# Kernel tuning notes

Measured on AMD Instinct MI355X. Metric: run time of the kernel, lower is better.

Reference implementation:

```python
import jax, jax.numpy as jnp
import numpy as np

N = 1_048_576   # collocation points
D_IN = 3        # seq_net[0]
H = 32          # hidden width (seq_net[1..3])
B = 4           # seq_net[-1] = number of parallel branches / outputs


def setup_inputs() -> dict:
    key = jax.random.key(0)
    ks = jax.random.split(key, 9)

    def init_w(k, shape, fan_in):
        bound = 1.0 / np.sqrt(fan_in)
        return jax.random.uniform(k, shape, jnp.float32, -bound, bound)

    x = jax.random.normal(ks[0], (N, D_IN), dtype=jnp.float32)
    # Per-branch weights stacked on leading branch axis B (torch.nn.Linear init ranges).
    W0 = init_w(ks[1], (B, D_IN, H), D_IN)
    b0 = init_w(ks[2], (B, H), D_IN)
    W1 = init_w(ks[3], (B, H, H), H)
    b1 = init_w(ks[4], (B, H), H)
    W2 = init_w(ks[5], (B, H, H), H)
    b2 = init_w(ks[6], (B, H), H)
    W3 = init_w(ks[7], (B, H, 1), H)
    b3 = init_w(ks[8], (B, 1), H)
    return {"x": x, "W0": W0, "b0": b0, "W1": W1, "b1": b1,
            "W2": W2, "b2": b2, "W3": W3, "b3": b3}


def reference(x, W0, b0, W1, b1, W2, b2, W3, b3):
    # All B branches computed as one batched GEMM chain (same math as the
    # python loop over per-branch Linear+tanh stacks in PFNN.forward).
    h = jnp.tanh(jnp.einsum('nd,bdh->bnh', x, W0) + b0[:, None, :])   # [B,N,H]
    h = jnp.tanh(jnp.einsum('bnd,bdh->bnh', h, W1) + b1[:, None, :])  # [B,N,H]
    h = jnp.tanh(jnp.einsum('bnd,bdh->bnh', h, W2) + b2[:, None, :])  # [B,N,H]
    out = jnp.einsum('bnd,bdh->bnh', h, W3) + b3[:, None, :]          # [B,N,1]
    # torch.cat(preds, dim=1): branch outputs side by side -> [N, B]
    return jnp.transpose(out[:, :, 0])
```

## Files before the change

kernel.cpp:

```cpp
#include <hip/hip_runtime.h>


#define NPTS 1048576
#define BLOCK 256
#define HROW 72
#define SCALE 2.8853900817779268f

#define OFF_BSC  16384
#define OFF_W0S  17408
#define OFF_B0S  18944
#define OFF_W3P  19456

using f16   = _Float16;
using f16x8 = __attribute__((ext_vector_type(8))) _Float16;
using f32x4 = __attribute__((ext_vector_type(4))) float;
using hfx2  = decltype(__builtin_amdgcn_cvt_pkrtz(0.0f, 0.0f));

__device__ __forceinline__ void tanh4_pre(float v0, float v1, float v2, float v3,
                                          float& o0, float& o1, float& o2, float& o3)
{
    float a0 = __builtin_amdgcn_exp2f(v0) + 1.0f;
    float a1 = __builtin_amdgcn_exp2f(v1) + 1.0f;
    float a2 = __builtin_amdgcn_exp2f(v2) + 1.0f;
    float a3 = __builtin_amdgcn_exp2f(v3) + 1.0f;
    float p01  = a0 * a1;
    float p012 = p01 * a2;
    float p    = p012 * a3;
    float r    = __builtin_amdgcn_rcpf(p);
    float inv3 = r * p012;
    float s    = r * a3;
    float inv2 = s * p01;
    float s2   = s * a2;
    float inv1 = s2 * a0;
    float inv0 = s2 * a1;
    o0 = __builtin_fmaf(-2.0f, inv0, 1.0f);
    o1 = __builtin_fmaf(-2.0f, inv1, 1.0f);
    o2 = __builtin_fmaf(-2.0f, inv2, 1.0f);
    o3 = __builtin_fmaf(-2.0f, inv3, 1.0f);
}

__global__ void prep_kernel(const float* __restrict__ W0, const float* __restrict__ b0,
                            const float* __restrict__ W1, const float* __restrict__ b1,
                            const float* __restrict__ W2, const float* __restrict__ b2,
                            const float* __restrict__ W3,
                            unsigned char* __restrict__ ws)
{
    int i = blockIdx.x * 256 + threadIdx.x;
    if (i < 8192) {
        int k = i & 31, n = (i >> 5) & 15, t = (i >> 9) & 1, b = (i >> 10) & 3, l = i >> 12;
        int f = 2 * n + t;
        const float* W = l ? W2 : W1;
        reinterpret_cast<f16*>(ws)[i] = (f16)(SCALE * W[(b * 32 + k) * 32 + f]);
    } else if (i < 8448) {
        int j = i - 8192;
        int n = j & 15, t = (j >> 4) & 1, b = (j >> 5) & 3, l = j >> 7;
        const float* bb = l ? b2 : b1;
        reinterpret_cast<float*>(ws + OFF_BSC)[j] = SCALE * bb[b * 32 + 2 * n + t];
    } else if (i < 8832) {
        int j = i - 8448;
        reinterpret_cast<float*>(ws + OFF_W0S)[j] = SCALE * W0[j];
    } else if (i < 8960) {
        int j = i - 8832;
        reinterpret_cast<float*>(ws + OFF_B0S)[j] = SCALE * b0[j];
    } else if (i < 9024) {
        int j = i - 8960;
        union { hfx2 h; unsigned int u; } cv;
        cv.h = __builtin_amdgcn_cvt_pkrtz(W3[2 * j], W3[2 * j + 1]);
        reinterpret_cast<unsigned int*>(ws + OFF_W3P)[j] = cv.u;
    }
}

__global__ __launch_bounds__(BLOCK) void pfnn_kernel(
    const float* __restrict__ x, const unsigned char* __restrict__ ws,
    const float* __restrict__ b3,
    float* __restrict__ out)
{
    __shared__ __align__(16) unsigned char Hl[4][64 * HROW];

    const f16*   Wf  = reinterpret_cast<const f16*>(ws);
    const float* Bsc = reinterpret_cast<const float*>(ws + OFF_BSC);
    const float* W0s = reinterpret_cast<const float*>(ws + OFF_W0S);
    const float* b0s = reinterpret_cast<const float*>(ws + OFF_B0S);
    const unsigned int* W3p = reinterpret_cast<const unsigned int*>(ws + OFF_W3P);

    const int t    = threadIdx.x;
    const int lane = t & 63;
    const int wv   = t >> 6;
    const int col  = lane & 15;
    const int quad = lane >> 4;
    unsigned char* __restrict__ H = &Hl[wv][0];

    const int n0 = blockIdx.x * BLOCK + t;
    const float x0 = x[3 * n0 + 0];
    const float x1 = x[3 * n0 + 1];
    const float x2 = x[3 * n0 + 2];

    float res[4];

    #pragma unroll 1
    for (int b = 0; b < 4; ++b) {
        {
            const float* __restrict__ w0  = W0s + b * 96;
            const float* __restrict__ bb0 = b0s + b * 32;
            unsigned char* row = H + lane * HROW;
            #pragma unroll
            for (int j = 0; j < 8; ++j) {
                float a[4];
                #pragma unroll
                for (int q = 0; q < 4; ++q) {
                    int f = 4 * j + q;
                    float v = bb0[f];
                    v = __builtin_fmaf(x0, w0[f],      v);
                    v = __builtin_fmaf(x1, w0[32 + f], v);
                    v = __builtin_fmaf(x2, w0[64 + f], v);
                    a[q] = v;
                }
                float o0, o1, o2, o3;
                tanh4_pre(a[0], a[1], a[2], a[3], o0, o1, o2, o3);
                union { hfx2 h; unsigned int u; } cv0, cv1;
                cv0.h = __builtin_amdgcn_cvt_pkrtz(o0, o1);
                cv1.h = __builtin_amdgcn_cvt_pkrtz(o2, o3);
                uint2 u; u.x = cv0.u; u.y = cv1.u;
                *reinterpret_cast<uint2*>(row + 8 * j) = u;
            }
        }

        #pragma unroll
        for (int l = 0; l < 2; ++l) {
            const f16* wb = Wf + ((l * 4 + b) * 2) * 512;
            f16x8 bf0 = *reinterpret_cast<const f16x8*>(wb + col * 32 + quad * 8);
            f16x8 bf1 = *reinterpret_cast<const f16x8*>(wb + 512 + col * 32 + quad * 8);
            float bias0 = Bsc[((l * 4 + b) * 2 + 0) * 16 + col];
            float bias1 = Bsc[((l * 4 + b) * 2 + 1) * 16 + col];

            f32x4 c[4][2];
            #pragma unroll
            for (int mt = 0; mt < 4; ++mt) {
                f32x4 c0 = {bias0, bias0, bias0, bias0};
                f32x4 c1 = {bias1, bias1, bias1, bias1};
                c[mt][0] = c0; c[mt][1] = c1;
            }
            #pragma unroll
            for (int mt = 0; mt < 4; ++mt) {
                const unsigned char* arow = H + (mt * 16 + col) * HROW + quad * 16;
                uint2 alo = *reinterpret_cast<const uint2*>(arow);
                uint2 ahi = *reinterpret_cast<const uint2*>(arow + 8);
                union { uint4 u; f16x8 f; } av;
                av.u = make_uint4(alo.x, alo.y, ahi.x, ahi.y);
                c[mt][0] = __builtin_amdgcn_mfma_f32_16x16x32_f16(av.f, bf0, c[mt][0], 0, 0, 0);
                c[mt][1] = __builtin_amdgcn_mfma_f32_16x16x32_f16(av.f, bf1, c[mt][1], 0, 0, 0);
            }
            #pragma unroll
            for (int mt = 0; mt < 4; ++mt) {
                #pragma unroll
                for (int r = 0; r < 4; r += 2) {
                    int p = mt * 16 + quad * 4 + r;
                    float o0, o1, o2, o3;
                    tanh4_pre(c[mt][0][r], c[mt][1][r],
                              c[mt][0][r + 1], c[mt][1][r + 1], o0, o1, o2, o3);
                    union { hfx2 h; unsigned int u; } cv0, cv1;
                    cv0.h = __builtin_amdgcn_cvt_pkrtz(o0, o1);
                    cv1.h = __builtin_amdgcn_cvt_pkrtz(o2, o3);
                    *reinterpret_cast<unsigned int*>(H + p * HROW + 4 * col)       = cv0.u;
                    *reinterpret_cast<unsigned int*>(H + (p + 1) * HROW + 4 * col) = cv1.u;
                }
            }
        }

        {
            float o = b3[b];
            const unsigned char* row = H + lane * HROW;
            const unsigned int* w3p = W3p + b * 16;
            #pragma unroll
            for (int i = 0; i < 8; ++i) {
                uint2 u = *reinterpret_cast<const uint2*>(row + 8 * i);
#if __has_builtin(__builtin_amdgcn_fdot2)
                union { unsigned int uu; hfx2 hh; } h0, h1, w0, w1;
                h0.uu = u.x; h1.uu = u.y;
                w0.uu = w3p[2 * i]; w1.uu = w3p[2 * i + 1];
                o = __builtin_amdgcn_fdot2(h0.hh, w0.hh, o, false);
                o = __builtin_amdgcn_fdot2(h1.hh, w1.hh, o, false);
#else
                union { unsigned int uu; f16 h[2]; } h0, h1, w0, w1;
                h0.uu = u.x; h1.uu = u.y;
                w0.uu = w3p[2 * i]; w1.uu = w3p[2 * i + 1];
                o = __builtin_fmaf((float)h0.h[0], (float)w0.h[0], o);
                o = __builtin_fmaf((float)h0.h[1], (float)w0.h[1], o);
                o = __builtin_fmaf((float)h1.h[0], (float)w1.h[0], o);
                o = __builtin_fmaf((float)h1.h[1], (float)w1.h[1], o);
#endif
            }
            res[b] = o;
        }
    }

    float4 r4 = make_float4(res[0], res[1], res[2], res[3]);
    *reinterpret_cast<float4*>(out + 4 * n0) = r4;
}

extern "C" void kernel_launch(void* const* d_in, const int* in_sizes, int n_in,
                              void* d_out, int out_size, void* d_ws, size_t ws_size,
                              hipStream_t stream) {
    const float* x  = (const float*)d_in[0];
    const float* W0 = (const float*)d_in[1];
    const float* b0 = (const float*)d_in[2];
    const float* W1 = (const float*)d_in[3];
    const float* b1 = (const float*)d_in[4];
    const float* W2 = (const float*)d_in[5];
    const float* b2 = (const float*)d_in[6];
    const float* W3 = (const float*)d_in[7];
    const float* b3 = (const float*)d_in[8];
    float* out = (float*)d_out;
    unsigned char* ws = (unsigned char*)d_ws;

    prep_kernel<<<dim3(36), dim3(256), 0, stream>>>(W0, b0, W1, b1, W2, b2, W3, ws);
    pfnn_kernel<<<dim3(NPTS / BLOCK), dim3(BLOCK), 0, stream>>>(x, ws, b3, out);
}
```

Baseline: 172.3 us.

## Move first layer (3->32) onto MFMA with split-fp16 inputs and weights

The per-thread scalar FMA computation of layer 0 is replaced with an MFMA. Inputs x are split into fp16 hi and lo parts, gathered across lanes with ds_bpermute into A fragments, and paired with a split-precision weight layout so that x_hi*w_hi + x_lo*w_hi + x_hi*w_lo keep roughly fp32 accuracy. This removes about 96 FMAs per branch per point and reuses the shared MFMA epilogue. The cost is extra bpermutes, a bigger prep kernel, and a possible small precision change.

Result: no change. 172.4 us (+0.1%).

```diff
diff --git a/kernel.cpp b/kernel.cpp
--- a/kernel.cpp
+++ b/kernel.cpp
@@ -7,9 +7,9 @@
 #define SCALE 2.8853900817779268f
 
 #define OFF_BSC  16384
-#define OFF_W0S  17408
-#define OFF_B0S  18944
-#define OFF_W3P  19456
+#define OFF_W0F  17408
+#define OFF_B0P  25600
+#define OFF_W3P  26112
 
 using f16   = _Float16;
 using f16x8 = __attribute__((ext_vector_type(8))) _Float16;
@@ -39,6 +39,27 @@
     o3 = __builtin_fmaf(-2.0f, inv3, 1.0f);
 }
 
+__device__ __forceinline__ void mfma_epilogue(const f32x4 (&c)[4][2],
+                                              unsigned char* __restrict__ H,
+                                              int col, int quad)
+{
+    #pragma unroll
+    for (int mt = 0; mt < 4; ++mt) {
+        #pragma unroll
+        for (int r = 0; r < 4; r += 2) {
+            int p = mt * 16 + quad * 4 + r;
+            float o0, o1, o2, o3;
+            tanh4_pre(c[mt][0][r], c[mt][1][r],
+                      c[mt][0][r + 1], c[mt][1][r + 1], o0, o1, o2, o3);
+            union { hfx2 h; unsigned int u; } cv0, cv1;
+            cv0.h = __builtin_amdgcn_cvt_pkrtz(o0, o1);
+            cv1.h = __builtin_amdgcn_cvt_pkrtz(o2, o3);
+            *reinterpret_cast<unsigned int*>(H + p * HROW + 4 * col)       = cv0.u;
+            *reinterpret_cast<unsigned int*>(H + (p + 1) * HROW + 4 * col) = cv1.u;
+        }
+    }
+}
+
 __global__ void prep_kernel(const float* __restrict__ W0, const float* __restrict__ b0,
                             const float* __restrict__ W1, const float* __restrict__ b1,
                             const float* __restrict__ W2, const float* __restrict__ b2,
@@ -56,14 +77,27 @@
         int n = j & 15, t = (j >> 4) & 1, b = (j >> 5) & 3, l = j >> 7;
         const float* bb = l ? b2 : b1;
         reinterpret_cast<float*>(ws + OFF_BSC)[j] = SCALE * bb[b * 32 + 2 * n + t];
-    } else if (i < 8832) {
+    } else if (i < 12544) {
         int j = i - 8448;
-        reinterpret_cast<float*>(ws + OFF_W0S)[j] = SCALE * W0[j];
-    } else if (i < 8960) {
-        int j = i - 8832;
-        reinterpret_cast<float*>(ws + OFF_B0S)[j] = SCALE * b0[j];
-    } else if (i < 9024) {
-        int j = i - 8960;
+        int k = j & 31, n = (j >> 5) & 15, t = (j >> 9) & 1, b = (j >> 10) & 3;
+        int f = 2 * n + t;
+        int q = k >> 3, jj = k & 7;
+        int row = -1; bool lo = false;
+        if (q == 0 && jj < 6)      row = (jj < 3) ? jj : jj - 3;
+        else if (q == 1 && jj < 3) { row = jj; lo = true; }
+        f16 outv = (f16)0.0f;
+        if (row >= 0) {
+            float w  = SCALE * W0[(b * 3 + row) * 32 + f];
+            f16   wh = (f16)w;
+            outv = lo ? (f16)(w - (float)wh) : wh;
+        }
+        reinterpret_cast<f16*>(ws + OFF_W0F)[((b * 2 + t) * 16 + n) * 32 + k] = outv;
+    } else if (i < 12672) {
+        int j = i - 12544;
+        int n = j & 15, t = (j >> 4) & 1, b = j >> 5;
+        reinterpret_cast<float*>(ws + OFF_B0P)[(b * 2 + t) * 16 + n] = SCALE * b0[b * 32 + 2 * n + t];
+    } else if (i < 12736) {
+        int j = i - 12672;
         union { hfx2 h; unsigned int u; } cv;
         cv.h = __builtin_amdgcn_cvt_pkrtz(W3[2 * j], W3[2 * j + 1]);
         reinterpret_cast<unsigned int*>(ws + OFF_W3P)[j] = cv.u;
@@ -79,8 +113,8 @@
 
     const f16*   Wf  = reinterpret_cast<const f16*>(ws);
     const float* Bsc = reinterpret_cast<const float*>(ws + OFF_BSC);
-    const float* W0s = reinterpret_cast<const float*>(ws + OFF_W0S);
-    const float* b0s = reinterpret_cast<const float*>(ws + OFF_B0S);
+    const f16*   W0f = reinterpret_cast<const f16*>(ws + OFF_W0F);
+    const float* B0p = reinterpret_cast<const float*>(ws + OFF_B0P);
     const unsigned int* W3p = reinterpret_cast<const unsigned int*>(ws + OFF_W3P);
 
     const int t    = threadIdx.x;
@@ -95,34 +129,52 @@
     const float x1 = x[3 * n0 + 1];
     const float x2 = x[3 * n0 + 2];
 
+    f16x8 xfrag[4];
+    {
+        union { hfx2 h; int u; } q0_, q1_, q2_;
+        q0_.h = __builtin_amdgcn_cvt_pkrtz(x0, x1);
+        float r0 = x0 - (float)q0_.h[0];
+        float r1 = x1 - (float)q0_.h[1];
+        q1_.h = __builtin_amdgcn_cvt_pkrtz(x2, r0);
+        float r2 = x2 - (float)q1_.h[0];
+        q2_.h = __builtin_amdgcn_cvt_pkrtz(r1, r2);
+        int d0 = q0_.u, d1 = q1_.u, d2 = q2_.u;
+        #pragma unroll
+        for (int mt = 0; mt < 4; ++mt) {
+            int addr = 4 * (mt * 16 + col);
+            union { int i[4]; f16x8 f; } u;
+            u.i[0] = __builtin_amdgcn_ds_bpermute(addr, d0);
+            u.i[1] = __builtin_amdgcn_ds_bpermute(addr, d1);
+            u.i[2] = __builtin_amdgcn_ds_bpermute(addr, d2);
+            u.i[3] = 0;
+            xfrag[mt] = u.f;
+        }
+    }
+
     float res[4];
 
     #pragma unroll 1
     for (int b = 0; b < 4; ++b) {
         {
-            const float* __restrict__ w0  = W0s + b * 96;
-            const float* __restrict__ bb0 = b0s + b * 32;
-            unsigned char* row = H + lane * HROW;
-            #pragma unroll
-            for (int j = 0; j < 8; ++j) {
-                float a[4];
-                #pragma unroll
-                for (int q = 0; q < 4; ++q) {
-                    int f = 4 * j + q;
-                    float v = bb0[f];
-                    v = __builtin_fmaf(x0, w0[f],      v);
-                    v = __builtin_fmaf(x1, w0[32 + f], v);
-                    v = __builtin_fmaf(x2, w0[64 + f], v);
-                    a[q] = v;
-                }
-                float o0, o1, o2, o3;
-                tanh4_pre(a[0], a[1], a[2], a[3], o0, o1, o2, o3);
-                union { hfx2 h; unsigned int u; } cv0, cv1;
-                cv0.h = __builtin_amdgcn_cvt_pkrtz(o0, o1);
-                cv1.h = __builtin_amdgcn_cvt_pkrtz(o2, o3);
-                uint2 u; u.x = cv0.u; u.y = cv1.u;
-                *reinterpret_cast<uint2*>(row + 8 * j) = u;
-            }
+            const f16* wb = W0f + (b * 2) * 512;
+            f16x8 bf0 = *reinterpret_cast<const f16x8*>(wb + col * 32 + quad * 8);
+            f16x8 bf1 = *reinterpret_cast<const f16x8*>(wb + 512 + col * 32 + quad * 8);
+            float bias0 = B0p[(b * 2 + 0) * 16 + col];
+            float bias1 = B0p[(b * 2 + 1) * 16 + col];
+
+            f32x4 c[4][2];
+            #pragma unroll
+            for (int mt = 0; mt < 4; ++mt) {
+                f32x4 c0 = {bias0, bias0, bias0, bias0};
+                f32x4 c1 = {bias1, bias1, bias1, bias1};
+                c[mt][0] = c0; c[mt][1] = c1;
+            }
+            #pragma unroll
+            for (int mt = 0; mt < 4; ++mt) {
+                c[mt][0] = __builtin_amdgcn_mfma_f32_16x16x32_f16(xfrag[mt], bf0, c[mt][0], 0, 0, 0);
+                c[mt][1] = __builtin_amdgcn_mfma_f32_16x16x32_f16(xfrag[mt], bf1, c[mt][1], 0, 0, 0);
+            }
+            mfma_epilogue(c, H, col, quad);
         }
 
         #pragma unroll
@@ -150,21 +202,7 @@
                 c[mt][0] = __builtin_amdgcn_mfma_f32_16x16x32_f16(av.f, bf0, c[mt][0], 0, 0, 0);
                 c[mt][1] = __builtin_amdgcn_mfma_f32_16x16x32_f16(av.f, bf1, c[mt][1], 0, 0, 0);
             }
-            #pragma unroll
-            for (int mt = 0; mt < 4; ++mt) {
-                #pragma unroll
-                for (int r = 0; r < 4; r += 2) {
-                    int p = mt * 16 + quad * 4 + r;
-                    float o0, o1, o2, o3;
-                    tanh4_pre(c[mt][0][r], c[mt][1][r],
-                              c[mt][0][r + 1], c[mt][1][r + 1], o0, o1, o2, o3);
-                    union { hfx2 h; unsigned int u; } cv0, cv1;
-                    cv0.h = __builtin_amdgcn_cvt_pkrtz(o0, o1);
-                    cv1.h = __builtin_amdgcn_cvt_pkrtz(o2, o3);
-                    *reinterpret_cast<unsigned int*>(H + p * HROW + 4 * col)       = cv0.u;
-                    *reinterpret_cast<unsigned int*>(H + (p + 1) * HROW + 4 * col) = cv1.u;
-                }
-            }
+            mfma_epilogue(c, H, col, quad);
         }
 
         {
@@ -213,6 +251,6 @@
     float* out = (float*)d_out;
     unsigned char* ws = (unsigned char*)d_ws;
 
-    prep_kernel<<<dim3(36), dim3(256), 0, stream>>>(W0, b0, W1, b1, W2, b2, W3, ws);
+    prep_kernel<<<dim3(50), dim3(256), 0, stream>>>(W0, b0, W1, b1, W2, b2, W3, ws);
     pfnn_kernel<<<dim3(NPTS / BLOCK), dim3(BLOCK), 0, stream>>>(x, ws, b3, out);
 }
```
